# Optimization experiments

Hardware: AMD Instinct MI355X
Metric: run time of the kernel (lower is better)

## Reference

```python
import jax, jax.numpy as jnp
import numpy as np

IMG = 224.0

def _recon_loss(pred, gt, vis):
    mask = vis.astype(bool)[..., None]  # [B,F,N,1]
    diff2 = jnp.where(mask, (pred - gt) ** 2, 0.0)
    count = jnp.sum(mask) * 3  # masked rows, 3 coords each
    valid = jnp.where(mask, gt, jnp.inf).reshape(-1, 3)
    min_vals = jnp.min(valid, axis=0)
    max_vals = jnp.max(jnp.where(mask, gt, -jnp.inf).reshape(-1, 3), axis=0)
    scale = jax.lax.stop_gradient(jnp.max(max_vals - min_vals) + 1e-6)
    return jnp.sum(diff2) / jnp.maximum(count, 1) / (scale ** 2)

def _identity_loss(pred, P, tracks):
    # pred [B,F,N,3], P [V,B,3,4], tracks [V,B,F,N,2]
    homo = jnp.concatenate([pred, jnp.ones(pred.shape[:-1] + (1,), pred.dtype)], axis=-1)
    # batched projection: one GEMM with K=4
    p2h = jnp.einsum('bfnk,vbjk->vbfnj', homo, P)  # [V,B,F,N,3]
    p2d = p2h[..., :2] / (p2h[..., 2:3] + 1e-10)
    dist = (p2d - tracks) ** 2 / IMG  # per-coordinate divide by 224
    # sum over (view, frame, batch) of mean over [N,2], / (V*F*B) == global mean
    return jnp.mean(dist)

def _temporal_loss(pred):
    vel = pred[:, 1:] - pred[:, :-1]
    acc = vel[:, 1:] - vel[:, :-1] if vel.shape[1] > 1 else vel
    tloss = jnp.mean(jnp.sum(acc ** 2, axis=-1))
    flat = pred.reshape(-1, 3)
    scale = jax.lax.stop_gradient(jnp.max(jnp.max(flat, 0) - jnp.min(flat, 0)) + 1e-6)
    return tloss / (scale ** 2)

def setup_inputs() -> dict:
    key = jax.random.key(0)
    k1, k2, k3, k4, k5 = jax.random.split(key, 5)
    B, F, N, V = 4, 512, 1024, 4
    return {
        'pred_points': jax.random.normal(k1, (B, F, N, 3), jnp.float32),
        'gt_points': jax.random.normal(k2, (B, F, N, 3), jnp.float32),
        'visibility': jax.random.randint(k3, (B, F, N), 0, 2, jnp.int32),
        'projection_matrices': jax.random.normal(k4, (V, B, 3, 4), jnp.float32),
        'tracks_2d': jax.random.uniform(k5, (V, B, F, N, 2), jnp.float32) * IMG,
    }

def reference(pred_points, gt_points, visibility, projection_matrices, tracks_2d):
    lam_id, lam_temp, lam_rec = 1.0, 0.5, 1.0
    recon = _recon_loss(pred_points, gt_points, visibility)
    ident = _identity_loss(pred_points, projection_matrices, tracks_2d)
    temp = _temporal_loss(pred_points)
    total = lam_rec * recon + lam_id * ident + lam_temp * temp
    return (total, recon, ident, temp)
```

## Files before the change

kernel.cpp:

```cpp
#include <hip/hip_runtime.h>
#include <math.h>

#define NTHR 256
#define CF   4
#define NBLK 2048
#define B_ 4
#define F_ 512
#define N_ 1024
#define V_ 4
#define NSLOT 5

struct Partial {
  float sum_diff2, sum_dist, sum_acc2, cnt;
  float gmin[3], gmax[3], pmin[3], pmax[3];
};

__device__ __forceinline__ void gl_lds16(const void* g, void* l) {
  __builtin_amdgcn_global_load_lds(
      (const __attribute__((address_space(1))) void*)g,
      (__attribute__((address_space(3))) void*)l, 16, 0, 0);
}

__global__ __launch_bounds__(NTHR) void loss_main(
    const float* __restrict__ pred, const float* __restrict__ gt,
    const int* __restrict__ vis, const float* __restrict__ P,
    const float* __restrict__ tracks, Partial* __restrict__ partials)
{
  __shared__ __align__(16) char sPred[NSLOT * 3072];
  __shared__ __align__(16) char sScr[1024];
  __shared__ Partial sw[NTHR / 64];

  const int bid = ((blockIdx.x & 7) << 8) | (blockIdx.x >> 3);
  const int b  = __builtin_amdgcn_readfirstlane(bid >> 9);
  const int fc = (bid >> 2) & 127;
  const int qr = bid & 3;
  const int f0 = fc << 2;
  const int n0 = qr << 8;
  const int t = threadIdx.x;
  const int wave = t >> 6, lane = t & 63;

  float Pmv[V_][12];
#pragma unroll
  for (int v = 0; v < V_; ++v)
#pragma unroll
    for (int j = 0; j < 12; ++j)
      Pmv[v][j] = P[(v * B_ + b) * 12 + j];

  for (int c = wave; c < 12; c += 4) {
    const char* src; char* dst;
    if (c < 9) {
      const int r = c / 3, k = c - r * 3;
      src = (const char*)pred +
          ((size_t)(b * F_ + f0 + r) * N_ + n0) * 12 + (k << 10) + lane * 16;
      dst = sPred + r * 3072 + (k << 10);
    } else {
      src = (const char*)pred + lane * 16;
      dst = sScr;
    }
    gl_lds16(src, dst);
  }

  float sum_diff2 = 0.0f, sum_dist = 0.0f, sum_acc2 = 0.0f, cntf = 0.0f;
  float gmin[3] = { INFINITY,  INFINITY,  INFINITY};
  float gmax[3] = {-INFINITY, -INFINITY, -INFINITY};
  float pmin[3] = { INFINITY,  INFINITY,  INFINITY};
  float pmax[3] = {-INFINITY, -INFINITY, -INFINITY};

#pragma unroll
  for (int i = 0; i < CF; ++i) {
    const int fi = f0 + i;
    const size_t ei = (size_t)(b * F_ + fi) * N_ + n0 + t;

    const float gx = gt[ei * 3], gy = gt[ei * 3 + 1], gz = gt[ei * 3 + 2];
    const int vm = vis[ei];
    const size_t fnt = ((size_t)fi << 10) + n0 + t;
    const float2 tk0 = *(const float2*)(tracks + ((((size_t)(0 * B_ + b) << 19) + fnt) << 1));
    const float2 tk1 = *(const float2*)(tracks + ((((size_t)(1 * B_ + b) << 19) + fnt) << 1));
    const float2 tk2 = *(const float2*)(tracks + ((((size_t)(2 * B_ + b) << 19) + fnt) << 1));
    const float2 tk3 = *(const float2*)(tracks + ((((size_t)(3 * B_ + b) << 19) + fnt) << 1));

    {
      const int rowPre = (fi + 3 < F_) ? fi + 3 : F_ - 1;
      const char* src; char* dst;
      if (wave < 3) {
        src = (const char*)pred +
            ((size_t)(b * F_ + rowPre) * N_ + n0) * 12 + (wave << 10) + lane * 16;
        dst = sPred + ((i + 3) % NSLOT) * 3072 + (wave << 10);
      } else {
        src = (const char*)pred + lane * 16;
        dst = sScr;
      }
      gl_lds16(src, dst);
    }

    asm volatile("s_waitcnt vmcnt(1) lgkmcnt(0)\n\ts_barrier" ::: "memory");

    const float* s0 = (const float*)(sPred + ((i    ) % NSLOT) * 3072) + 3 * t;
    const float* s1 = (const float*)(sPred + ((i + 1) % NSLOT) * 3072) + 3 * t;
    const float* s2 = (const float*)(sPred + ((i + 2) % NSLOT) * 3072) + 3 * t;
    const float px = s0[0], py = s0[1], pz = s0[2];

    pmin[0] = fminf(pmin[0], px); pmax[0] = fmaxf(pmax[0], px);
    pmin[1] = fminf(pmin[1], py); pmax[1] = fmaxf(pmax[1], py);
    pmin[2] = fminf(pmin[2], pz); pmax[2] = fmaxf(pmax[2], pz);

    const float vmf = vm ? 1.0f : 0.0f;
    const float d0 = px - gx, d1 = py - gy, d2 = pz - gz;
    sum_diff2 += vmf * (d0 * d0 + d1 * d1 + d2 * d2);
    cntf += vmf;
    gmin[0] = fminf(gmin[0], vm ? gx :  INFINITY);
    gmax[0] = fmaxf(gmax[0], vm ? gx : -INFINITY);
    gmin[1] = fminf(gmin[1], vm ? gy :  INFINITY);
    gmax[1] = fmaxf(gmax[1], vm ? gy : -INFINITY);
    gmin[2] = fminf(gmin[2], vm ? gz :  INFINITY);
    gmax[2] = fmaxf(gmax[2], vm ? gz : -INFINITY);

    const float am = (fi < F_ - 2) ? 1.0f : 0.0f;
    const float a0 = s2[0] - 2.0f * s1[0] + px;
    const float a1 = s2[1] - 2.0f * s1[1] + py;
    const float a2 = s2[2] - 2.0f * s1[2] + pz;
    sum_acc2 += am * (a0 * a0 + a1 * a1 + a2 * a2);

    const float2 tks[V_] = {tk0, tk1, tk2, tk3};
#pragma unroll
    for (int v = 0; v < V_; ++v) {
      const float h0 = Pmv[v][0] * px + Pmv[v][1] * py + Pmv[v][2]  * pz + Pmv[v][3];
      const float h1 = Pmv[v][4] * px + Pmv[v][5] * py + Pmv[v][6]  * pz + Pmv[v][7];
      const float h2 = Pmv[v][8] * px + Pmv[v][9] * py + Pmv[v][10] * pz + Pmv[v][11];
      const float inv = __builtin_amdgcn_rcpf(h2 + 1e-10f);
      const float dx = h0 * inv - tks[v].x;
      const float dy = h1 * inv - tks[v].y;
      sum_dist += dx * dx + dy * dy;
    }
  }

#pragma unroll
  for (int o = 32; o > 0; o >>= 1) {
    sum_diff2 += __shfl_down(sum_diff2, o);
    sum_dist  += __shfl_down(sum_dist,  o);
    sum_acc2  += __shfl_down(sum_acc2,  o);
    cntf      += __shfl_down(cntf,      o);
#pragma unroll
    for (int k = 0; k < 3; ++k) {
      gmin[k] = fminf(gmin[k], __shfl_down(gmin[k], o));
      gmax[k] = fmaxf(gmax[k], __shfl_down(gmax[k], o));
      pmin[k] = fminf(pmin[k], __shfl_down(pmin[k], o));
      pmax[k] = fmaxf(pmax[k], __shfl_down(pmax[k], o));
    }
  }

  if (lane == 0) {
    Partial p;
    p.sum_diff2 = sum_diff2; p.sum_dist = sum_dist;
    p.sum_acc2  = sum_acc2;  p.cnt      = cntf;
#pragma unroll
    for (int k = 0; k < 3; ++k) {
      p.gmin[k] = gmin[k]; p.gmax[k] = gmax[k];
      p.pmin[k] = pmin[k]; p.pmax[k] = pmax[k];
    }
    sw[wave] = p;
  }
  __syncthreads();
  if (t == 0) {
    Partial p = sw[0];
#pragma unroll
    for (int w = 1; w < NTHR / 64; ++w) {
      p.sum_diff2 += sw[w].sum_diff2; p.sum_dist += sw[w].sum_dist;
      p.sum_acc2  += sw[w].sum_acc2;  p.cnt      += sw[w].cnt;
#pragma unroll
      for (int k = 0; k < 3; ++k) {
        p.gmin[k] = fminf(p.gmin[k], sw[w].gmin[k]);
        p.gmax[k] = fmaxf(p.gmax[k], sw[w].gmax[k]);
        p.pmin[k] = fminf(p.pmin[k], sw[w].pmin[k]);
        p.pmax[k] = fmaxf(p.pmax[k], sw[w].pmax[k]);
      }
    }
    partials[bid] = p;
  }
}

__global__ __launch_bounds__(NTHR) void loss_final(
    const Partial* __restrict__ partials, float* __restrict__ out)
{
  float sum_diff2 = 0.0f, sum_dist = 0.0f, sum_acc2 = 0.0f, cnt = 0.0f;
  float gmin[3] = { INFINITY,  INFINITY,  INFINITY};
  float gmax[3] = {-INFINITY, -INFINITY, -INFINITY};
  float pmin[3] = { INFINITY,  INFINITY,  INFINITY};
  float pmax[3] = {-INFINITY, -INFINITY, -INFINITY};

  const int tid = threadIdx.x;
  for (int i = tid; i < NBLK; i += NTHR) {
    const Partial p = partials[i];
    sum_diff2 += p.sum_diff2; sum_dist += p.sum_dist;
    sum_acc2  += p.sum_acc2;  cnt      += p.cnt;
#pragma unroll
    for (int k = 0; k < 3; ++k) {
      gmin[k] = fminf(gmin[k], p.gmin[k]); gmax[k] = fmaxf(gmax[k], p.gmax[k]);
      pmin[k] = fminf(pmin[k], p.pmin[k]); pmax[k] = fmaxf(pmax[k], p.pmax[k]);
    }
  }

#pragma unroll
  for (int o = 32; o > 0; o >>= 1) {
    sum_diff2 += __shfl_down(sum_diff2, o);
    sum_dist  += __shfl_down(sum_dist,  o);
    sum_acc2  += __shfl_down(sum_acc2,  o);
    cnt       += __shfl_down(cnt,       o);
#pragma unroll
    for (int k = 0; k < 3; ++k) {
      gmin[k] = fminf(gmin[k], __shfl_down(gmin[k], o));
      gmax[k] = fmaxf(gmax[k], __shfl_down(gmax[k], o));
      pmin[k] = fminf(pmin[k], __shfl_down(pmin[k], o));
      pmax[k] = fmaxf(pmax[k], __shfl_down(pmax[k], o));
    }
  }

  __shared__ Partial sw[NTHR / 64];
  const int lane = tid & 63;
  const int wave = tid >> 6;
  if (lane == 0) {
    Partial p;
    p.sum_diff2 = sum_diff2; p.sum_dist = sum_dist;
    p.sum_acc2  = sum_acc2;  p.cnt      = cnt;
#pragma unroll
    for (int k = 0; k < 3; ++k) {
      p.gmin[k] = gmin[k]; p.gmax[k] = gmax[k];
      p.pmin[k] = pmin[k]; p.pmax[k] = pmax[k];
    }
    sw[wave] = p;
  }
  __syncthreads();

  if (tid == 0) {
    Partial p = sw[0];
#pragma unroll
    for (int w = 1; w < NTHR / 64; ++w) {
      p.sum_diff2 += sw[w].sum_diff2; p.sum_dist += sw[w].sum_dist;
      p.sum_acc2  += sw[w].sum_acc2;  p.cnt      += sw[w].cnt;
#pragma unroll
      for (int k = 0; k < 3; ++k) {
        p.gmin[k] = fminf(p.gmin[k], sw[w].gmin[k]);
        p.gmax[k] = fmaxf(p.gmax[k], sw[w].gmax[k]);
        p.pmin[k] = fminf(p.pmin[k], sw[w].pmin[k]);
        p.pmax[k] = fmaxf(p.pmax[k], sw[w].pmax[k]);
      }
    }

    double sr = -INFINITY;
#pragma unroll
    for (int k = 0; k < 3; ++k) sr = fmax(sr, (double)p.gmax[k] - (double)p.gmin[k]);
    sr += 1e-6;
    const double recon = (double)p.sum_diff2 / fmax((double)p.cnt * 3.0, 1.0) / (sr * sr);

    const double ident = (double)p.sum_dist / 224.0 / ((double)V_ * B_ * F_ * N_ * 2.0);

    double st = -INFINITY;
#pragma unroll
    for (int k = 0; k < 3; ++k) st = fmax(st, (double)p.pmax[k] - (double)p.pmin[k]);
    st += 1e-6;
    const double tloss = (double)p.sum_acc2 / ((double)B_ * (F_ - 2) * N_);
    const double temp = tloss / (st * st);

    const double total = recon + ident + 0.5 * temp;
    out[0] = (float)total;
    out[1] = (float)recon;
    out[2] = (float)ident;
    out[3] = (float)temp;
  }
}

extern "C" void kernel_launch(void* const* d_in, const int* in_sizes, int n_in,
                              void* d_out, int out_size, void* d_ws, size_t ws_size,
                              hipStream_t stream) {
  const float* pred   = (const float*)d_in[0];
  const float* gt     = (const float*)d_in[1];
  const int*   vis    = (const int*)d_in[2];
  const float* P      = (const float*)d_in[3];
  const float* tracks = (const float*)d_in[4];
  float* out = (float*)d_out;
  Partial* partials = (Partial*)d_ws;

  loss_main<<<NBLK, NTHR, 0, stream>>>(pred, gt, vis, P, tracks, partials);
  loss_final<<<1, NTHR, 0, stream>>>(partials, out);
}
```

Before: 35.33 us.

## Prefetch gt/vis into LDS and register-prefetch tracks one frame ahead

Moves the gt and visibility loads into a double-buffered LDS staging area using async global-to-LDS loads issued one frame ahead, and software-pipelines the four per-view track loads in registers one iteration ahead. The waitcnt threshold is raised so the current frame's data is ready while the next frame's loads stay in flight. The aim is to hide global memory latency in this bandwidth-bound reduction. The cost is extra LDS use, more live registers, and one redundant clamped load at the final frame. The hand-set vmcnt count has to match the actual load ordering exactly, or the kernel could read data before it arrives.

```diff
diff --git a/kernel.cpp b/kernel.cpp
--- a/kernel.cpp
+++ b/kernel.cpp
@@ -27,6 +27,7 @@
     const float* __restrict__ tracks, Partial* __restrict__ partials)
 {
   __shared__ __align__(16) char sPred[NSLOT * 3072];
+  __shared__ __align__(16) char sCons[2 * 4096];
   __shared__ __align__(16) char sScr[1024];
   __shared__ Partial sw[NTHR / 64];
 
@@ -59,6 +60,23 @@
     }
     gl_lds16(src, dst);
   }
+  {
+    const char* src; char* dst;
+    if (wave < 3) {
+      src = (const char*)gt +
+          ((size_t)(b * F_ + f0) * N_ + n0) * 12 + (wave << 10) + lane * 16;
+      dst = sCons + (wave << 10);
+    } else {
+      src = (const char*)vis + ((size_t)(b * F_ + f0) * N_ + n0) * 4 + lane * 16;
+      dst = sCons + 3072;
+    }
+    gl_lds16(src, dst);
+  }
+  size_t fntc = ((size_t)f0 << 10) + n0 + t;
+  float2 tk0c = *(const float2*)(tracks + ((((size_t)(0 * B_ + b) << 19) + fntc) << 1));
+  float2 tk1c = *(const float2*)(tracks + ((((size_t)(1 * B_ + b) << 19) + fntc) << 1));
+  float2 tk2c = *(const float2*)(tracks + ((((size_t)(2 * B_ + b) << 19) + fntc) << 1));
+  float2 tk3c = *(const float2*)(tracks + ((((size_t)(3 * B_ + b) << 19) + fntc) << 1));
 
   float sum_diff2 = 0.0f, sum_dist = 0.0f, sum_acc2 = 0.0f, cntf = 0.0f;
   float gmin[3] = { INFINITY,  INFINITY,  INFINITY};
@@ -69,15 +87,27 @@
 #pragma unroll
   for (int i = 0; i < CF; ++i) {
     const int fi = f0 + i;
-    const size_t ei = (size_t)(b * F_ + fi) * N_ + n0 + t;
-
-    const float gx = gt[ei * 3], gy = gt[ei * 3 + 1], gz = gt[ei * 3 + 2];
-    const int vm = vis[ei];
-    const size_t fnt = ((size_t)fi << 10) + n0 + t;
-    const float2 tk0 = *(const float2*)(tracks + ((((size_t)(0 * B_ + b) << 19) + fnt) << 1));
-    const float2 tk1 = *(const float2*)(tracks + ((((size_t)(1 * B_ + b) << 19) + fnt) << 1));
-    const float2 tk2 = *(const float2*)(tracks + ((((size_t)(2 * B_ + b) << 19) + fnt) << 1));
-    const float2 tk3 = *(const float2*)(tracks + ((((size_t)(3 * B_ + b) << 19) + fnt) << 1));
+    const int fn1 = (fi + 1 < F_) ? fi + 1 : F_ - 1;
+
+    const size_t fntn = ((size_t)fn1 << 10) + n0 + t;
+    const float2 tk0n = *(const float2*)(tracks + ((((size_t)(0 * B_ + b) << 19) + fntn) << 1));
+    const float2 tk1n = *(const float2*)(tracks + ((((size_t)(1 * B_ + b) << 19) + fntn) << 1));
+    const float2 tk2n = *(const float2*)(tracks + ((((size_t)(2 * B_ + b) << 19) + fntn) << 1));
+    const float2 tk3n = *(const float2*)(tracks + ((((size_t)(3 * B_ + b) << 19) + fntn) << 1));
+
+    {
+      const char* src; char* dst;
+      char* cd = sCons + ((i + 1) & 1) * 4096;
+      if (wave < 3) {
+        src = (const char*)gt +
+            ((size_t)(b * F_ + fn1) * N_ + n0) * 12 + (wave << 10) + lane * 16;
+        dst = cd + (wave << 10);
+      } else {
+        src = (const char*)vis + ((size_t)(b * F_ + fn1) * N_ + n0) * 4 + lane * 16;
+        dst = cd + 3072;
+      }
+      gl_lds16(src, dst);
+    }
 
     {
       const int rowPre = (fi + 3 < F_) ? fi + 3 : F_ - 1;
@@ -93,12 +123,16 @@
       gl_lds16(src, dst);
     }
 
-    asm volatile("s_waitcnt vmcnt(1) lgkmcnt(0)\n\ts_barrier" ::: "memory");
+    asm volatile("s_waitcnt vmcnt(6) lgkmcnt(0)\n\ts_barrier" ::: "memory");
 
     const float* s0 = (const float*)(sPred + ((i    ) % NSLOT) * 3072) + 3 * t;
     const float* s1 = (const float*)(sPred + ((i + 1) % NSLOT) * 3072) + 3 * t;
     const float* s2 = (const float*)(sPred + ((i + 2) % NSLOT) * 3072) + 3 * t;
+    const char* cc = sCons + (i & 1) * 4096;
+    const float* sG = (const float*)cc + 3 * t;
+    const int   vm  = ((const int*)(cc + 3072))[t];
     const float px = s0[0], py = s0[1], pz = s0[2];
+    const float gx = sG[0], gy = sG[1], gz = sG[2];
 
     pmin[0] = fminf(pmin[0], px); pmax[0] = fmaxf(pmax[0], px);
     pmin[1] = fminf(pmin[1], py); pmax[1] = fmaxf(pmax[1], py);
@@ -121,7 +155,7 @@
     const float a2 = s2[2] - 2.0f * s1[2] + pz;
     sum_acc2 += am * (a0 * a0 + a1 * a1 + a2 * a2);
 
-    const float2 tks[V_] = {tk0, tk1, tk2, tk3};
+    const float2 tks[V_] = {tk0c, tk1c, tk2c, tk3c};
 #pragma unroll
     for (int v = 0; v < V_; ++v) {
       const float h0 = Pmv[v][0] * px + Pmv[v][1] * py + Pmv[v][2]  * pz + Pmv[v][3];
@@ -132,6 +166,8 @@
       const float dy = h1 * inv - tks[v].y;
       sum_dist += dx * dx + dy * dy;
     }
+
+    tk0c = tk0n; tk1c = tk1n; tk2c = tk2n; tk3c = tk3n;
   }
 
 #pragma unroll
```

Measured after the change: 36.68 us. 3.8% more time.
